# Kernel optimization log

Hardware: AMD Instinct MI355X
Metric: run time of the kernel (lower is better)

The kernel has to match this reference:

```python
import jax, jax.numpy as jnp
import numpy as np

B, N, D = 4, 2048, 512
OUT, H = 512, 8
HD = OUT // H

def setup_inputs() -> dict:
    key = jax.random.key(0)
    ks = jax.random.split(key, 10)
    s = 1.0 / np.sqrt(D)
    x = jax.random.normal(ks[0], (B, N, D), dtype=jnp.float32)
    adj = jax.random.randint(ks[1], (N, N), 0, 2, dtype=jnp.int32)
    Wq = jax.random.uniform(ks[2], (D, OUT), jnp.float32, -s, s)
    bq = jax.random.uniform(ks[3], (OUT,), jnp.float32, -s, s)
    Wk = jax.random.uniform(ks[4], (D, OUT), jnp.float32, -s, s)
    bk = jax.random.uniform(ks[5], (OUT,), jnp.float32, -s, s)
    Wv = jax.random.uniform(ks[6], (D, OUT), jnp.float32, -s, s)
    bv = jax.random.uniform(ks[7], (OUT,), jnp.float32, -s, s)
    so = 1.0 / np.sqrt(OUT)
    Wo = jax.random.uniform(ks[8], (OUT, OUT), jnp.float32, -so, so)
    bo = jax.random.uniform(ks[9], (OUT,), jnp.float32, -so, so)
    return {"x": x, "adj": adj, "Wq": Wq, "bq": bq, "Wk": Wk, "bk": bk,
            "Wv": Wv, "bv": bv, "Wo": Wo, "bo": bo}

def reference(x, adj, Wq, bq, Wk, bk, Wv, bv, Wo, bo):
    scale = HD ** -0.5
    # [B,N,OUT] -> [B,H,N,HD]
    def split_heads(t):
        return t.reshape(B, N, H, HD).transpose(0, 2, 1, 3)
    q = split_heads(x @ Wq + bq)
    k = split_heads(x @ Wk + bk)
    v = split_heads(x @ Wv + bv)
    attn = jnp.einsum('bhnd,bhmd->bhnm', q, k) * scale  # [B,H,N,N]
    mask = (adj == 0)[None, None, :, :]
    attn = jnp.where(mask, jnp.float32(-1e9), attn)
    attn = jax.nn.softmax(attn, axis=-1)
    out = jnp.einsum('bhnm,bhmd->bhnd', attn, v)
    out = out.transpose(0, 2, 1, 3).reshape(B, N, OUT)
    return out @ Wo + bo
```

## Files before the change

### kernel.cpp

```cpp
#include <hip/hip_runtime.h>
#include <math.h>

#define NB   4
#define NN   2048
#define DD   512
#define NOUT 512
#define NH   8
#define HDIM 64

typedef __attribute__((ext_vector_type(4))) short bf16x4;
typedef __attribute__((ext_vector_type(8))) short bf16x8;
typedef __attribute__((ext_vector_type(4))) float f32x4;
#define MFMA32(a, b, c)  __builtin_amdgcn_mfma_f32_16x16x32_bf16(a, b, c, 0, 0, 0)

typedef const __attribute__((address_space(1))) unsigned int* gas_ptr;
typedef __attribute__((address_space(3))) unsigned int* las_ptr;

#define SCALE2 0.18033688f


__device__ inline unsigned short f2bf(float f) {
    unsigned int u = __float_as_uint(f);
    u += 0x7fffu + ((u >> 16) & 1u);
    return (unsigned short)(u >> 16);
}

__device__ inline unsigned int pack_trunc(float lo, float hi) {
    return __builtin_amdgcn_perm(__float_as_uint(hi), __float_as_uint(lo), 0x07060302u);
}

#if __has_builtin(__builtin_amdgcn_exp2f)
#define EXP2(x) __builtin_amdgcn_exp2f(x)
#else
#define EXP2(x) exp2f(x)
#endif

#define SWZB(g) ((g) ^ (((g) >> 3) & 7))

__global__ __launch_bounds__(256) void prep(
    const float* __restrict__ x, unsigned short* __restrict__ xt,
    const float* __restrict__ W0, const float* __restrict__ W1,
    const float* __restrict__ W2, const float* __restrict__ W3,
    unsigned short* __restrict__ Tqkv, unsigned short* __restrict__ To,
    const int* __restrict__ adj, unsigned int* __restrict__ amaskW)
{
    const int blk = blockIdx.x;
    const int t   = threadIdx.x;

    if (blk < 2048) {
        const int i = (blk * 256 + t) * 8;
        const int m = i >> 9, k = i & 511;
        float4 a = *(const float4*)(x + i);
        float4 b = *(const float4*)(x + i + 4);
        ushort4 u0, u1;
        u0.x = f2bf(a.x); u0.y = f2bf(a.y); u0.z = f2bf(a.z); u0.w = f2bf(a.w);
        u1.x = f2bf(b.x); u1.y = f2bf(b.y); u1.z = f2bf(b.z); u1.w = f2bf(b.w);
        unsigned short* dst = xt + ((size_t)(m >> 7) * 65536)
                                 + (k >> 5) * 4096 + (m & 127) * 32 + (k & 31);
        *(ushort4*)dst       = u0;
        *(ushort4*)(dst + 4) = u1;
        return;
    }
    if (blk < 2304) {
        __shared__ float tile[64][65];
        const int idx = blk - 2048;
        const int z = idx >> 6, rem = idx & 63;
        const float* W;
        switch (z) {
            case 0:  W = W0; break;
            case 1:  W = W1; break;
            case 2:  W = W2; break;
            default: W = W3; break;
        }
        unsigned short* T = (z < 3) ? Tqkv : To;
        const int ngbase  = (z < 3) ? z * 512 : 0;
        const int k0 = (rem & 7) * 64, n0 = (rem >> 3) * 64;
        const int r = t >> 6, c = t & 63;
#pragma unroll
        for (int rep = 0; rep < 16; ++rep) {
            const int row = rep * 4 + r;
            tile[row][c] = W[(size_t)(k0 + row) * NOUT + n0 + c];
        }
        __syncthreads();
        const int k  = k0 + c;
        const int ks = k >> 5, kk = k & 31;
#pragma unroll
        for (int rep = 0; rep < 16; ++rep) {
            const int row = rep * 4 + r;
            const int ng  = ngbase + n0 + row;
            T[((size_t)(ng >> 7) * 65536) + ks * 4096 + (ng & 127) * 32 + kk]
                = f2bf(tile[c][row]);
        }
        return;
    }
    {
        const int gid  = (blk - 2304) * 256 + t;
        const int w0   = gid * 4;
        const int qrow = w0 >> 10;
        const int wloc = w0 & 1023;
        const int kb0  = wloc * 2;
        int4 a0 = *(const int4*)(adj + (size_t)qrow * NN + kb0);
        int4 a1 = *(const int4*)(adj + (size_t)qrow * NN + kb0 + 4);
        uint4 m;
        m.x = (a0.x ? 0xFFFFu : 0u) | (a0.y ? 0xFFFF0000u : 0u);
        m.y = (a0.z ? 0xFFFFu : 0u) | (a0.w ? 0xFFFF0000u : 0u);
        m.z = (a1.x ? 0xFFFFu : 0u) | (a1.y ? 0xFFFF0000u : 0u);
        m.w = (a1.z ? 0xFFFFu : 0u) | (a1.w ? 0xFFFF0000u : 0u);
        *(uint4*)(amaskW + (size_t)qrow * 1024 + wloc) = m;
    }
}

#define GTS_STAGE(ks, Ab, Bb, NB16)                                            \
    {                                                                          \
        const unsigned short* As_ = Asrc + (ks) * 4096;                        \
        const unsigned short* Bs_ = Bsrc + (ks) * 4096;                        \
        __builtin_amdgcn_global_load_lds(                                      \
            (gas_ptr)(As_ + (wave * 64 + lswz) * 8),                           \
            (las_ptr)((Ab) + wave * 512), 16, 0, 0);                           \
        __builtin_amdgcn_global_load_lds(                                      \
            (gas_ptr)(As_ + (256 + wave * 64 + lswz) * 8),                     \
            (las_ptr)((Ab) + 2048 + wave * 512), 16, 0, 0);                    \
        __builtin_amdgcn_global_load_lds(                                      \
            (gas_ptr)(Bs_ + (wave * 64 + lswz) * 8),                           \
            (las_ptr)((Bb) + wave * 512), 16, 0, 0);                           \
        if ((NB16) == 512)                                                     \
            __builtin_amdgcn_global_load_lds(                                  \
                (gas_ptr)(Bs_ + (256 + wave * 64 + lswz) * 8),                 \
                (las_ptr)((Bb) + 2048 + wave * 512), 16, 0, 0);                \
    }

#define GT_MFMA(Af, Bf, NTC)                                                   \
    _Pragma("unroll")                                                          \
    for (int mt = 0; mt < 4; ++mt)                                             \
        _Pragma("unroll")                                                      \
        for (int nt = 0; nt < NTC; ++nt)                                       \
            acc[mt][nt] = MFMA32(Af[mt], Bf[nt], acc[mt][nt]);

#define GTS_FRAGS(Ab, Bb, NTC)                                                 \
    bf16x8 aF[4], bF[NTC];                                                     \
    _Pragma("unroll")                                                          \
    for (int mt = 0; mt < 4; ++mt) aF[mt] = *(const bf16x8*)&(Ab)[aOff[mt]];   \
    _Pragma("unroll")                                                          \
    for (int nt = 0; nt < NTC; ++nt) bF[nt] = *(const bf16x8*)&(Bb)[bOff[nt]];

#define GTS_LOOP(NTC, NB16, sA0, sB0, sA1, sB1)                                \
    const int lswz = lane ^ ((lane >> 3) & 7);                                 \
    int aOff[4], bOff[NTC];                                                    \
    _Pragma("unroll")                                                          \
    for (int mt = 0; mt < 4; ++mt)                                             \
        aOff[mt] = SWZB((wm + mt * 16 + l16) * 4 + quad) * 8;                  \
    _Pragma("unroll")                                                          \
    for (int nt = 0; nt < NTC; ++nt)                                           \
        bOff[nt] = SWZB((wn + nt * 16 + l16) * 4 + quad) * 8;                  \
    f32x4 acc[4][NTC];                                                         \
    _Pragma("unroll")                                                          \
    for (int mt = 0; mt < 4; ++mt)                                             \
        _Pragma("unroll")                                                      \
        for (int nt = 0; nt < NTC; ++nt) acc[mt][nt] = (f32x4){0.f, 0.f, 0.f, 0.f}; \
    GTS_STAGE(0, sA0, sB0, NB16);                                              \
    for (int kk = 0; kk < 8; ++kk) {                                           \
        __syncthreads();                                                       \
        GTS_STAGE(2 * kk + 1, sA1, sB1, NB16);                                 \
        { GTS_FRAGS(sA0, sB0, NTC); GT_MFMA(aF, bF, NTC); }                    \
        __syncthreads();                                                       \
        if (kk < 7) GTS_STAGE(2 * kk + 2, sA0, sB0, NB16);                     \
        { GTS_FRAGS(sA1, sB1, NTC); GT_MFMA(aF, bF, NTC); }                    \
    }

__global__ __launch_bounds__(256, 3) void gemm_qkv(
    const unsigned short* __restrict__ Atil,
    const unsigned short* __restrict__ Wtil,
    const float* __restrict__ bq, const float* __restrict__ bk,
    const float* __restrict__ bv,
    unsigned short* __restrict__ qo, unsigned short* __restrict__ ko,
    unsigned short* __restrict__ vto)
{
    __shared__ unsigned short smem[16384];
    unsigned short* sA0 = smem;
    unsigned short* sB0 = smem + 4096;
    unsigned short* sA1 = smem + 8192;
    unsigned short* sB1 = smem + 12288;

    const int t = threadIdx.x, wave = t >> 6, lane = t & 63;
    const int quad = lane >> 4, l16 = lane & 15;
    const int n0 = blockIdx.x * 128, m0 = blockIdx.y * 128;
    const int wm = (wave & 1) * 64, wn = (wave >> 1) * 64;
    const unsigned short* Asrc = Atil + (size_t)blockIdx.y * 65536;
    const unsigned short* Bsrc = Wtil + (size_t)blockIdx.x * 65536;

    GTS_LOOP(4, 512, sA0, sB0, sA1, sB1);

    const int seg   = n0 >> 9;
    const int nloc0 = n0 & 511;
    const float* bp = (seg == 0) ? bq : (seg == 1) ? bk : bv;
    unsigned short* dst3 = (seg == 0) ? qo : (seg == 1) ? ko : vto;
    const int h = (nloc0 + wn) >> 6;

    float bias4[4];
#pragma unroll
    for (int nt = 0; nt < 4; ++nt) bias4[nt] = bp[nloc0 + wn + nt * 16 + l16];

    __syncthreads();
    unsigned short* Lo = smem + wave * 2560;
#pragma unroll
    for (int mt = 0; mt < 4; ++mt) {
        if (seg < 2) {
#pragma unroll
            for (int nt = 0; nt < 4; ++nt)
#pragma unroll
                for (int r = 0; r < 4; ++r) {
                    float val = acc[mt][nt][r] + bias4[nt];
                    if (seg == 0) val *= SCALE2;
                    Lo[(quad * 4 + r) * 72 + nt * 16 + l16] = f2bf(val);
                }
#pragma unroll
            for (int pass = 0; pass < 2; ++pass) {
                const int row = pass * 8 + (lane >> 3);
                const int mg  = m0 + wm + mt * 16 + row;
                const int bb  = mg >> 11, n = mg & (NN - 1);
                bf16x8 v = *(const bf16x8*)&Lo[row * 72 + (lane & 7) * 8];
                *(bf16x8*)(dst3 + ((size_t)(bb * NH + h) * NN + n) * HDIM
                           + (lane & 7) * 8) = v;
            }
        } else {
#pragma unroll
            for (int nt = 0; nt < 4; ++nt)
#pragma unroll
                for (int r = 0; r < 4; ++r) {
                    const float val = acc[mt][nt][r] + bias4[nt];
                    Lo[(nt * 16 + l16) * 40 + quad * 4 + r] = f2bf(val);
                }
            const int d  = lane;
            const int mg = m0 + wm + mt * 16;
            const int bb = mg >> 11, n = mg & (NN - 1);
            unsigned short* dr = dst3 + ((size_t)(bb * NH + h) * HDIM + d) * NN + n;
            *(bf16x8*)dr       = *(const bf16x8*)&Lo[d * 40];
            *(bf16x8*)(dr + 8) = *(const bf16x8*)&Lo[d * 40 + 8];
        }
    }
}

__global__ __launch_bounds__(256, 3) void gemm_o(
    const unsigned short* __restrict__ Atil,
    const unsigned short* __restrict__ Wtil,
    const float* __restrict__ bias,
    float* __restrict__ C)
{
    __shared__ unsigned short smem[12288];
    unsigned short* sA0 = smem;
    unsigned short* sB0 = smem + 4096;
    unsigned short* sA1 = smem + 6144;
    unsigned short* sB1 = smem + 10240;

    const int t = threadIdx.x, wave = t >> 6, lane = t & 63;
    const int quad = lane >> 4, l16 = lane & 15;
    const int n0 = blockIdx.x * 64, m0 = blockIdx.y * 128;
    const int wm = (wave & 1) * 64, wn = (wave >> 1) * 32;
    const unsigned short* Asrc = Atil + (size_t)blockIdx.y * 65536;
    const unsigned short* Bsrc = Wtil + (size_t)(n0 >> 7) * 65536 + (n0 & 64) * 32;

    GTS_LOOP(2, 256, sA0, sB0, sA1, sB1);

    float bias2[2];
#pragma unroll
    for (int nt = 0; nt < 2; ++nt) bias2[nt] = bias[n0 + wn + nt * 16 + l16];

#pragma unroll
    for (int mt = 0; mt < 4; ++mt)
#pragma unroll
        for (int nt = 0; nt < 2; ++nt) {
            const int col = n0 + wn + nt * 16 + l16;
#pragma unroll
            for (int r = 0; r < 4; ++r) {
                const int row = m0 + wm + mt * 16 + quad * 4 + r;
                C[(size_t)row * NOUT + col] = acc[mt][nt][r] + bias2[nt];
            }
        }
}

__global__ __launch_bounds__(512, 4) void attn_mfma(
    const unsigned short* __restrict__ qg,
    const unsigned short* __restrict__ kg,
    const unsigned short* __restrict__ vt,
    const unsigned int* __restrict__ amask,
    unsigned short* __restrict__ aot)
{
    __shared__ unsigned short smem[18432];
    unsigned short* Ka = smem;
    unsigned short* Va = smem + 4096;
    unsigned short* Kb = smem + 8192;
    unsigned short* Vb = smem + 12288;

    const int t    = threadIdx.x;
    const int wave = t >> 6;
    const int lane = t & 63;
    const int quad = lane >> 4;
    const int l16  = lane & 15;
    const int pair = wave >> 1;
    const int hk   = wave & 1;

    const int qt = blockIdx.x, h = blockIdx.y, b = blockIdx.z;
    const int bh = b * NH + h;
    const int q0 = qt * 128;

    const unsigned short* kbase  = kg + (size_t)bh * NN * HDIM;
    const unsigned short* vtbase = vt + (size_t)bh * HDIM * NN;

    const int drow = lane >> 3;
    const int dblk = (lane & 7) ^ drow;
    const int p  = wave * 8 + drow;
    const int Lp = (p & 32) + ((p >> 2) & 3) * 8 + ((p >> 4) & 1) * 4 + (p & 3);

    const int sw  = l16 & 7;
    const int bo0 = (quad ^ sw) * 8;
    const int bo1 = bo0 ^ 32;

#define ATT_ISSUE(kt, Kd, Vd)                                                  \
    {                                                                          \
        const int r0 = wave * 8;                                               \
        __builtin_amdgcn_global_load_lds(                                      \
            (gas_ptr)(kbase + (size_t)((kt) * 64 + Lp) * HDIM + dblk * 8),     \
            (las_ptr)(Kd + r0 * 64), 16, 0, 0);                                \
        __builtin_amdgcn_global_load_lds(                                      \
            (gas_ptr)(vtbase + (size_t)(r0 + drow) * NN + (kt) * 64 + dblk * 8), \
            (las_ptr)(Vd + r0 * 64), 16, 0, 0);                                \
    }

    const int myq0 = q0 + pair * 32 + l16;
    const int myq1 = myq0 + 16;
    const unsigned short* qrow0 = qg + ((size_t)bh * NN + myq0) * HDIM;
    const unsigned short* qrow1 = qg + ((size_t)bh * NN + myq1) * HDIM;
    const bf16x8 bQ0g0 = *(const bf16x8*)(qrow0 + quad * 8);
    const bf16x8 bQ1g0 = *(const bf16x8*)(qrow0 + quad * 8 + 32);
    const bf16x8 bQ0g1 = *(const bf16x8*)(qrow1 + quad * 8);
    const bf16x8 bQ1g1 = *(const bf16x8*)(qrow1 + quad * 8 + 32);

    const unsigned int* mrow0 = amask + (size_t)myq0 * 1024 + quad * 4;
    const unsigned int* mrow1 = amask + (size_t)myq1 * 1024 + quad * 4;
#define MLOAD(kt, g) (*(const uint4*)(((g) ? mrow1 : mrow0) + (kt) * 32 + hk * 16))

    bf16x8 ones8;
#pragma unroll
    for (int j = 0; j < 8; ++j) ones8[j] = (short)0x3F80;

    f32x4 O[4][2];
#pragma unroll
    for (int dt = 0; dt < 4; ++dt)
#pragma unroll
        for (int g = 0; g < 2; ++g) O[dt][g] = (f32x4){0.f, 0.f, 0.f, 0.f};
    f32x4 lacc[2];
    lacc[0] = (f32x4){0.f, 0.f, 0.f, 0.f};
    lacc[1] = (f32x4){0.f, 0.f, 0.f, 0.f};

    auto tile = [&](const unsigned short* Ks, const unsigned short* Vs,
                    uint4 mwg0, uint4 mwg1) {
        bf16x8 aK[2][2];
#pragma unroll
        for (int kg = 0; kg < 2; ++kg) {
            const int nt = hk * 2 + kg;
            aK[kg][0] = *(const bf16x8*)&Ks[(nt * 16 + l16) * 64 + bo0];
            aK[kg][1] = *(const bf16x8*)&Ks[(nt * 16 + l16) * 64 + bo1];
        }
        bf16x8 Pt[2];
#pragma unroll
        for (int g = 0; g < 2; ++g) {
            const uint4 mw = g ? mwg1 : mwg0;
            const bf16x8 q0f = g ? bQ0g1 : bQ0g0;
            const bf16x8 q1f = g ? bQ1g1 : bQ1g0;
            union { unsigned int u[4]; bf16x8 v; } cv;
#pragma unroll
            for (int kg = 0; kg < 2; ++kg) {
                f32x4 s = (f32x4){0.f, 0.f, 0.f, 0.f};
                s = MFMA32(aK[kg][0], q0f, s);
                s = MFMA32(aK[kg][1], q1f, s);
                const float p0 = EXP2(s[0]);
                const float p1 = EXP2(s[1]);
                const float p2 = EXP2(s[2]);
                const float p3 = EXP2(s[3]);
                cv.u[kg * 2 + 0] = pack_trunc(p0, p1) & (kg ? mw.z : mw.x);
                cv.u[kg * 2 + 1] = pack_trunc(p2, p3) & (kg ? mw.w : mw.y);
            }
            Pt[g] = cv.v;
            lacc[g] = MFMA32(ones8, Pt[g], lacc[g]);
        }
#pragma unroll
        for (int dt = 0; dt < 4; ++dt) {
            bf16x8 aV = *(const bf16x8*)
                &Vs[(dt * 16 + l16) * 64 + (((hk * 4 + quad) ^ sw) * 8)];
#pragma unroll
            for (int g = 0; g < 2; ++g)
                O[dt][g] = MFMA32(aV, Pt[g], O[dt][g]);
        }
    };

    uint4 mA0 = MLOAD(0, 0), mA1 = MLOAD(0, 1);
    uint4 mB0, mB1;
    ATT_ISSUE(0, Ka, Va);
    for (int kk = 0; kk < 16; ++kk) {
        __syncthreads();
        ATT_ISSUE(2 * kk + 1, Kb, Vb);
        mB0 = MLOAD(2 * kk + 1, 0); mB1 = MLOAD(2 * kk + 1, 1);
        tile(Ka, Va, mA0, mA1);
        __syncthreads();
        if (kk < 15) {
            ATT_ISSUE(2 * kk + 2, Ka, Va);
            mA0 = MLOAD(2 * kk + 2, 0); mA1 = MLOAD(2 * kk + 2, 1);
        }
        tile(Kb, Vb, mB0, mB1);
    }
    __syncthreads();

    float* F   = (float*)smem;
    float* myF = F + ((size_t)pair * 64 + lane) * 36;
    if (hk == 1) {
#pragma unroll
        for (int dt = 0; dt < 4; ++dt)
#pragma unroll
            for (int g = 0; g < 2; ++g)
                *(f32x4*)(myF + dt * 8 + g * 4) = O[dt][g];
        myF[32] = lacc[0][0];
        myF[33] = lacc[1][0];
    }
    __syncthreads();
    float inv0 = 0.f, inv1 = 0.f;
    if (hk == 0) {
#pragma unroll
        for (int dt = 0; dt < 4; ++dt)
#pragma unroll
            for (int g = 0; g < 2; ++g) {
                const f32x4 o2 = *(const f32x4*)(myF + dt * 8 + g * 4);
                O[dt][g] += o2;
            }
        inv0 = 1.f / (lacc[0][0] + myF[32]);
        inv1 = 1.f / (lacc[1][0] + myF[33]);
    }
    __syncthreads();

    if (hk == 0) {
#pragma unroll
        for (int g = 0; g < 2; ++g) {
            const float inv = g ? inv1 : inv0;
            unsigned short* Lo = smem + (pair * 2 + g) * 1152;
#pragma unroll
            for (int dt = 0; dt < 4; ++dt) {
                const float v0 = O[dt][g][0] * inv, v1 = O[dt][g][1] * inv;
                const float v2 = O[dt][g][2] * inv, v3 = O[dt][g][3] * inv;
                *(unsigned int*)&Lo[l16 * 72 + dt * 16 + quad * 4]     = pack_trunc(v0, v1);
                *(unsigned int*)&Lo[l16 * 72 + dt * 16 + quad * 4 + 2] = pack_trunc(v2, v3);
            }
            const int rr = lane >> 2;
            const int qq = q0 + pair * 32 + g * 16 + rr;
            const int m  = b * NN + qq;
            const int mb = m >> 7, r = m & 127;
#pragma unroll
            for (int i = 0; i < 2; ++i) {
                const int ch = (lane & 3) + 4 * i;
                const int ks = h * 2 + (ch >> 2);
                bf16x8 val = *(const bf16x8*)&Lo[rr * 72 + ch * 8];
                *(bf16x8*)(aot + (size_t)mb * 65536 + ks * 4096 + r * 32 + (ch & 3) * 8) = val;
            }
        }
    }
#undef ATT_ISSUE
#undef MLOAD
}

extern "C" void kernel_launch(void* const* d_in, const int* in_sizes, int n_in,
                              void* d_out, int out_size, void* d_ws, size_t ws_size,
                              hipStream_t stream)
{
    const float* x   = (const float*)d_in[0];
    const int*   adj = (const int*)  d_in[1];
    const float* Wq  = (const float*)d_in[2];
    const float* bq  = (const float*)d_in[3];
    const float* Wk  = (const float*)d_in[4];
    const float* bk  = (const float*)d_in[5];
    const float* Wv  = (const float*)d_in[6];
    const float* bv  = (const float*)d_in[7];
    const float* Wo  = (const float*)d_in[8];
    const float* bo  = (const float*)d_in[9];
    float* out = (float*)d_out;

    const size_t qkv_elems = (size_t)NB * NH * NN * HDIM;
    unsigned short* xt    = (unsigned short*)d_ws;
    unsigned short* q     = xt   + qkv_elems;
    unsigned short* kb    = q    + qkv_elems;
    unsigned short* vtb   = kb   + qkv_elems;
    unsigned short* tWqkv = vtb  + qkv_elems;
    unsigned short* tWo   = tWqkv + (size_t)3 * DD * NOUT;
    unsigned int*   amaskW = (unsigned int*)(tWo + (size_t)DD * NOUT);
    unsigned short* aot   = xt;

    prep<<<dim3(4352), 256, 0, stream>>>(x, xt, Wq, Wk, Wv, Wo,
                                         tWqkv, tWo, adj, amaskW);

    gemm_qkv<<<dim3(12, 64), 256, 0, stream>>>(xt, tWqkv, bq, bk, bv, q, kb, vtb);

    attn_mfma<<<dim3(NN / 128, NH, NB), 512, 0, stream>>>(q, kb, vtb, amaskW, aot);

    gemm_o<<<dim3(8, 64), 256, 0, stream>>>(aot, tWo, bo, out);
}
```

Before: 174.0 us.

## Move adj-mask and Wo conversion from prep into extra gemm_qkv blocks

The adjacency-to-bitmask conversion and the Wo transpose/bf16 conversion are taken out of the prep kernel and run as extra blocks (blockIdx.y >= 64) of the QKV GEMM launch. The aim is to shrink the serial prep kernel so that work the QKV GEMM does not depend on overlaps with the GEMM blocks. The trade-off is a larger GEMM grid where cheap memory-bound blocks compete with the MFMA tiles for CUs, and block scheduling order decides how much overlap actually happens.

```diff
diff --git a/kernel.cpp b/kernel.cpp
--- a/kernel.cpp
+++ b/kernel.cpp
@@ -40,9 +40,8 @@
 __global__ __launch_bounds__(256) void prep(
     const float* __restrict__ x, unsigned short* __restrict__ xt,
     const float* __restrict__ W0, const float* __restrict__ W1,
-    const float* __restrict__ W2, const float* __restrict__ W3,
-    unsigned short* __restrict__ Tqkv, unsigned short* __restrict__ To,
-    const int* __restrict__ adj, unsigned int* __restrict__ amaskW)
+    const float* __restrict__ W2,
+    unsigned short* __restrict__ Tqkv)
 {
     const int blk = blockIdx.x;
     const int t   = threadIdx.x;
@@ -61,19 +60,12 @@
         *(ushort4*)(dst + 4) = u1;
         return;
     }
-    if (blk < 2304) {
+    {
         __shared__ float tile[64][65];
         const int idx = blk - 2048;
         const int z = idx >> 6, rem = idx & 63;
-        const float* W;
-        switch (z) {
-            case 0:  W = W0; break;
-            case 1:  W = W1; break;
-            case 2:  W = W2; break;
-            default: W = W3; break;
-        }
-        unsigned short* T = (z < 3) ? Tqkv : To;
-        const int ngbase  = (z < 3) ? z * 512 : 0;
+        const float* W = (z == 0) ? W0 : (z == 1) ? W1 : W2;
+        const int ngbase = z * 512;
         const int k0 = (rem & 7) * 64, n0 = (rem >> 3) * 64;
         const int r = t >> 6, c = t & 63;
 #pragma unroll
@@ -88,25 +80,9 @@
         for (int rep = 0; rep < 16; ++rep) {
             const int row = rep * 4 + r;
             const int ng  = ngbase + n0 + row;
-            T[((size_t)(ng >> 7) * 65536) + ks * 4096 + (ng & 127) * 32 + kk]
+            Tqkv[((size_t)(ng >> 7) * 65536) + ks * 4096 + (ng & 127) * 32 + kk]
                 = f2bf(tile[c][row]);
         }
-        return;
-    }
-    {
-        const int gid  = (blk - 2304) * 256 + t;
-        const int w0   = gid * 4;
-        const int qrow = w0 >> 10;
-        const int wloc = w0 & 1023;
-        const int kb0  = wloc * 2;
-        int4 a0 = *(const int4*)(adj + (size_t)qrow * NN + kb0);
-        int4 a1 = *(const int4*)(adj + (size_t)qrow * NN + kb0 + 4);
-        uint4 m;
-        m.x = (a0.x ? 0xFFFFu : 0u) | (a0.y ? 0xFFFF0000u : 0u);
-        m.y = (a0.z ? 0xFFFFu : 0u) | (a0.w ? 0xFFFF0000u : 0u);
-        m.z = (a1.x ? 0xFFFFu : 0u) | (a1.y ? 0xFFFF0000u : 0u);
-        m.w = (a1.z ? 0xFFFFu : 0u) | (a1.w ? 0xFFFF0000u : 0u);
-        *(uint4*)(amaskW + (size_t)qrow * 1024 + wloc) = m;
     }
 }
 
@@ -173,9 +149,53 @@
     const float* __restrict__ bq, const float* __restrict__ bk,
     const float* __restrict__ bv,
     unsigned short* __restrict__ qo, unsigned short* __restrict__ ko,
-    unsigned short* __restrict__ vto)
+    unsigned short* __restrict__ vto,
+    const int* __restrict__ adj, unsigned int* __restrict__ amaskW,
+    const float* __restrict__ Wo, unsigned short* __restrict__ To)
 {
     __shared__ unsigned short smem[16384];
+
+    if (blockIdx.y >= 64) {
+        const int id = (blockIdx.y - 64) * 12 + blockIdx.x;
+        const int t  = threadIdx.x;
+        if (id < 2048) {
+            const int gid  = id * 256 + t;
+            const int w0   = gid * 4;
+            const int qrow = w0 >> 10;
+            const int wloc = w0 & 1023;
+            const int kb0  = wloc * 2;
+            int4 a0 = *(const int4*)(adj + (size_t)qrow * NN + kb0);
+            int4 a1 = *(const int4*)(adj + (size_t)qrow * NN + kb0 + 4);
+            uint4 m;
+            m.x = (a0.x ? 0xFFFFu : 0u) | (a0.y ? 0xFFFF0000u : 0u);
+            m.y = (a0.z ? 0xFFFFu : 0u) | (a0.w ? 0xFFFF0000u : 0u);
+            m.z = (a1.x ? 0xFFFFu : 0u) | (a1.y ? 0xFFFF0000u : 0u);
+            m.w = (a1.z ? 0xFFFFu : 0u) | (a1.w ? 0xFFFF0000u : 0u);
+            *(uint4*)(amaskW + (size_t)qrow * 1024 + wloc) = m;
+        } else {
+            float* tile = (float*)smem;
+            const int rem = id - 2048;
+            const int k0 = (rem & 7) * 64, n0 = (rem >> 3) * 64;
+            const int r = t >> 6, c = t & 63;
+#pragma unroll
+            for (int rep = 0; rep < 16; ++rep) {
+                const int row = rep * 4 + r;
+                tile[row * 65 + c] = Wo[(size_t)(k0 + row) * NOUT + n0 + c];
+            }
+            __syncthreads();
+            const int k  = k0 + c;
+            const int ks = k >> 5, kk = k & 31;
+#pragma unroll
+            for (int rep = 0; rep < 16; ++rep) {
+                const int row = rep * 4 + r;
+                const int ng  = n0 + row;
+                To[((size_t)(ng >> 7) * 65536) + ks * 4096 + (ng & 127) * 32 + kk]
+                    = f2bf(tile[c * 65 + row]);
+            }
+        }
+        return;
+    }
+
     unsigned short* sA0 = smem;
     unsigned short* sB0 = smem + 4096;
     unsigned short* sA1 = smem + 8192;
@@ -491,10 +511,10 @@
     unsigned int*   amaskW = (unsigned int*)(tWo + (size_t)DD * NOUT);
     unsigned short* aot   = xt;
 
-    prep<<<dim3(4352), 256, 0, stream>>>(x, xt, Wq, Wk, Wv, Wo,
-                                         tWqkv, tWo, adj, amaskW);
-
-    gemm_qkv<<<dim3(12, 64), 256, 0, stream>>>(xt, tWqkv, bq, bk, bv, q, kb, vtb);
+    prep<<<dim3(2240), 256, 0, stream>>>(x, xt, Wq, Wk, Wv, tWqkv);
+
+    gemm_qkv<<<dim3(12, 240), 256, 0, stream>>>(xt, tWqkv, bq, bk, bv, q, kb, vtb,
+                                                adj, amaskW, Wo, tWo);
 
     attn_mfma<<<dim3(NN / 128, NH, NB), 512, 0, stream>>>(q, kb, vtb, amaskW, aot);
 
```

Measured after the change: 175.8 us. No clear change (+1.0%).
